# Optimization experiments

Measured on AMD Instinct MI355X. Metric: run time of the kernel, lower is better.

Reference implementation:

```python
import jax, jax.numpy as jnp
import numpy as np

B, C, H, W = 16, 512, 32, 32

def _conv2d(x, w, b, pad):
    y = jax.lax.conv_general_dilated(
        x, w, window_strides=(1, 1), padding=[(pad, pad), (pad, pad)],
        dimension_numbers=('NCHW', 'OIHW', 'NCHW'))
    return y + b[None, :, None, None]

def setup_inputs() -> dict:
    key = jax.random.key(0)
    ks = jax.random.split(key, 10)
    s3 = 1.0 / np.sqrt(C * 9)   # torch conv2d default init scale (3x3)
    s1 = 1.0 / np.sqrt(3 * C)   # 1x1 conv over 3C input channels
    return {
        'x':  jax.random.normal(ks[0], (B, C, H, W), jnp.float32),
        'w1': jax.random.uniform(ks[1], (C, C, 3, 3), jnp.float32, -s3, s3),
        'b1': jax.random.uniform(ks[2], (C,), jnp.float32, -s3, s3),
        'w2': jax.random.uniform(ks[3], (C, C, 3, 3), jnp.float32, -s3, s3),
        'b2': jax.random.uniform(ks[4], (C,), jnp.float32, -s3, s3),
        'w3': jax.random.uniform(ks[5], (C, C, 3, 3), jnp.float32, -s3, s3),
        'b3': jax.random.uniform(ks[6], (C,), jnp.float32, -s3, s3),
        'alpha': jax.random.normal(ks[7], (), jnp.float32) * 0.1,
        'beta':  jax.random.normal(ks[8], (), jnp.float32) * 0.1,
        'wf': jax.random.uniform(ks[9], (C, 3 * C, 1, 1), jnp.float32, -s1, s1),
        'bf': jnp.zeros((C,), jnp.float32),
    }

def reference(x, w1, b1, w2, b2, w3, b3, alpha, beta, wf, bf):
    b, c, h, w = x.shape
    n = h * w
    # --- spatial attention ---
    A = _conv2d(x, w1, b1, 1).reshape(b, c, n)  # [b,C,N]
    Bm = _conv2d(x, w2, b2, 1).reshape(b, c, n)
    D = _conv2d(x, w3, b3, 1).reshape(b, c, n)
    M = jnp.einsum('bcn,bcm->bnm', A, Bm)       # A^T @ B, [b,N,N]
    M = jax.nn.softmax(M, axis=-1)
    # weighted_C = M @ D^T -> [b,N,C]; then permute to [b,C,N]
    spat = jnp.einsum('bnm,bcm->bcn', M, D).reshape(b, c, h, w)
    spat = alpha * spat
    # --- channel attention ---
    Xr = x.reshape(b, c, n)                     # [b,C,N]
    S = jnp.einsum('bcn,bdn->bcd', Xr, Xr)      # [b,C,C]
    S = jax.nn.softmax(S, axis=-1)
    # weighted = S^T @ Xr
    chan = jnp.einsum('bdc,bdn->bcn', S, Xr).reshape(b, c, h, w)
    chan = beta * chan
    # --- fuse ---
    cat = jnp.concatenate((x, spat, chan), axis=1)  # [b,3C,H,W]
    return _conv2d(cat, wf, bf, 0)
```

## Files before the change

kernel.cpp:

```cpp
#include <hip/hip_runtime.h>
#include <hip/hip_bf16.h>
#include <stdint.h>

#define B_   16
#define C_   512
#define N_   1024
#define C3   1536

using bf16x8 = __attribute__((ext_vector_type(8))) __bf16;
using f32x4  = __attribute__((ext_vector_type(4))) float;
typedef unsigned short ushort_t;

__device__ __forceinline__ ushort_t f2bf(float f) {
    union { float f; uint32_t u; } v; v.f = f;
    uint32_t r = v.u + 0x7FFFu + ((v.u >> 16) & 1u);
    return (ushort_t)(r >> 16);
}

typedef __attribute__((address_space(3))) void lds_void_t;
typedef const __attribute__((address_space(1))) void g_void_t;
__device__ __forceinline__ void gload16(const void* g, void* l) {
    __builtin_amdgcn_global_load_lds((g_void_t*)g, (lds_void_t*)l, 16, 0, 0);
}


__global__ void castwf_kernel(const float* __restrict__ wf,
                              ushort_t* __restrict__ Wfb,
                              ushort_t* __restrict__ zp,
                              const float* __restrict__ b1,
                              const float* __restrict__ b2,
                              const float* __restrict__ b3,
                              float* __restrict__ b_all) {
    int idx = blockIdx.x * 256 + threadIdx.x;
    if (idx < 512) zp[idx] = 0;
    if (idx < 1536) b_all[idx] = (idx < 512) ? b1[idx] : (idx < 1024) ? b2[idx - 512] : b3[idx - 1024];
    Wfb[idx] = f2bf(wf[idx]);
}

__global__ void castw_kernel(const float* __restrict__ w,
                             ushort_t* __restrict__ Wall, int coff) {
    int idx = blockIdx.x * 256 + threadIdx.x;
    int t = idx / (C_ * C_);
    int rem = idx - t * (C_ * C_);
    Wall[(size_t)t * (C3 * C_) + (size_t)coff * C_ + rem] = f2bf(w[(size_t)rem * 9 + t]);
}

__global__ void castx_kernel(const float* __restrict__ x,
                             ushort_t* __restrict__ Xb,
                             ushort_t* __restrict__ cat) {
    __shared__ ushort_t t[32][33];
    int n0 = blockIdx.x * 32, c0 = blockIdx.y * 32, b = blockIdx.z;
    int tx = threadIdx.x & 31, ty = threadIdx.x >> 5;
    const float* xb = x + ((size_t)b * C_ + c0) * N_ + n0;
#pragma unroll
    for (int q = 0; q < 4; ++q) {
        int c = ty + q * 8;
        ushort_t h = f2bf(xb[(size_t)c * N_ + tx]);
        Xb[((size_t)b * C_ + c0 + c) * N_ + n0 + tx] = h;
        t[c][tx] = h;
    }
    __syncthreads();
#pragma unroll
    for (int q = 0; q < 4; ++q) {
        int n = ty + q * 8;
        cat[((size_t)b * N_ + n0 + n) * C3 + c0 + tx] = t[tx][n];
    }
}

__global__ void transp_kernel(const ushort_t* __restrict__ Y,
                              ushort_t* __restrict__ Db) {
    __shared__ ushort_t t[32][33];
    int n0 = blockIdx.x * 32, c0 = blockIdx.y * 32, b = blockIdx.z;
    int tx = threadIdx.x & 31, ty = threadIdx.x >> 5;
#pragma unroll
    for (int q = 0; q < 4; ++q) {
        int n = ty + q * 8;
        t[n][tx] = Y[((size_t)b * N_ + n0 + n) * C3 + 1024 + c0 + tx];
    }
    __syncthreads();
#pragma unroll
    for (int q = 0; q < 4; ++q) {
        int c = ty + q * 8;
        Db[((size_t)b * C_ + c0 + c) * N_ + n0 + tx] = t[tx][c];
    }
}

__global__ void softmax_kernel(float* __restrict__ Mb) {
    int n = blockIdx.x, b = blockIdx.y;
    float* row = Mb + ((size_t)b * N_ + n) * N_;
    int tid = threadIdx.x;
    float4 v = ((const float4*)row)[tid];
    float m = fmaxf(fmaxf(v.x, v.y), fmaxf(v.z, v.w));
#pragma unroll
    for (int off = 1; off < 64; off <<= 1) m = fmaxf(m, __shfl_xor(m, off));
    __shared__ float sm[4], ss[4];
    int wid = tid >> 6, lane = tid & 63;
    if (lane == 0) sm[wid] = m;
    __syncthreads();
    m = fmaxf(fmaxf(sm[0], sm[1]), fmaxf(sm[2], sm[3]));
    float e0 = __expf(v.x - m), e1 = __expf(v.y - m);
    float e2 = __expf(v.z - m), e3 = __expf(v.w - m);
    float s = e0 + e1 + e2 + e3;
#pragma unroll
    for (int off = 1; off < 64; off <<= 1) s += __shfl_xor(s, off);
    if (lane == 0) ss[wid] = s;
    __syncthreads();
    s = ss[0] + ss[1] + ss[2] + ss[3];
    float r = 1.0f / s;
    ushort4 o;
    o.x = f2bf(e0 * r); o.y = f2bf(e1 * r); o.z = f2bf(e2 * r); o.w = f2bf(e3 * r);
    ((ushort4*)row)[tid] = o;
}

__global__ void rowstats_kernel(const float* __restrict__ S,
                                float* __restrict__ mxv, float* __restrict__ rzv) {
    int c = blockIdx.x, b = blockIdx.y;
    const float* row = S + ((size_t)b * C_ + c) * C_;
    int tid = threadIdx.x;
    float2 v = ((const float2*)row)[tid];
    float m = fmaxf(v.x, v.y);
#pragma unroll
    for (int off = 1; off < 64; off <<= 1) m = fmaxf(m, __shfl_xor(m, off));
    __shared__ float sm[4], ss[4];
    int wid = tid >> 6, lane = tid & 63;
    if (lane == 0) sm[wid] = m;
    __syncthreads();
    m = fmaxf(fmaxf(sm[0], sm[1]), fmaxf(sm[2], sm[3]));
    float e = __expf(v.x - m) + __expf(v.y - m);
#pragma unroll
    for (int off = 1; off < 64; off <<= 1) e += __shfl_xor(e, off);
    if (lane == 0) ss[wid] = e;
    __syncthreads();
    if (tid == 0) {
        e = ss[0] + ss[1] + ss[2] + ss[3];
        mxv[(size_t)b * C_ + c] = m;
        rzv[(size_t)b * C_ + c] = 1.0f / e;
    }
}

__global__ void sst_kernel(const float* __restrict__ S,
                           const float* __restrict__ mxv, const float* __restrict__ rzv,
                           ushort_t* __restrict__ Sst) {
    int idx = blockIdx.x * 256 + threadIdx.x;
    int d = idx & (C_ - 1);
    int b = idx >> 18;
    float st = mxv[((size_t)b << 9) + d];
    float rz = rzv[((size_t)b << 9) + d];
    Sst[idx] = f2bf(__expf(S[idx] - st) * rz);
}

#define BM 128
#define BN 128
#define BKk 64

template <int XMODE, int OUTF32, int BIASMODE, int SCALE, int SWZ>
__global__ __launch_bounds__(256)
void gemm_bt_kernel(const ushort_t* __restrict__ Ab, int lda, long long strideA, long long tapA,
                    const ushort_t* __restrict__ Bb, int ldb, long long strideB, long long tapB,
                    void* __restrict__ Cb, int ldc, long long strideC,
                    int K, int ntaps,
                    const float* __restrict__ bias,
                    const float* __restrict__ scaleptr,
                    const ushort_t* __restrict__ zpage) {
    __shared__ short As[BM * BKk];
    __shared__ short Bs[BN * BKk];
    int tid = threadIdx.x;
    int wid = tid >> 6, lane = tid & 63;
    int wr = wid >> 1, wc = wid & 1;
    int j0, i0, b;
    if (SWZ) {
        int bid = blockIdx.x;
        int swz = (bid & 7) * 192 + (bid >> 3);
        j0 = (swz >> 7) * BN;
        i0 = (swz & 127) * BM;
        b = 0;
    } else {
        j0 = blockIdx.x * BN; i0 = blockIdx.y * BM; b = blockIdx.z;
    }
    const ushort_t* Abase = Ab + (size_t)b * strideA;
    const ushort_t* Bbase = Bb + (size_t)b * strideB;

    f32x4 acc[4][4] = {};

    int rs = wid * 32 + (lane >> 3);
    int kb = (lane & 7) * 8;

    for (int tap = 0; tap < ntaps; ++tap) {
        const ushort_t* At_ = Abase + (size_t)tap * tapA;
        const ushort_t* Bt_ = Bbase + (size_t)tap * tapB;
        const ushort_t* aq[4];
        const ushort_t* bq[4];
        if (XMODE == 1) {
            int dh = tap / 3 - 1, dw = tap - (tap / 3) * 3 - 1;
            int nshift = dh * 32 + dw;
#pragma unroll
            for (int q = 0; q < 4; ++q) {
                int n = i0 + rs + q * 8;
                int nn = n & (N_ - 1);
                int hh = (nn >> 5) + dh, ww = (nn & 31) + dw;
                bool valid = ((unsigned)hh < 32u) && ((unsigned)ww < 32u);
                aq[q] = valid ? (At_ + (size_t)(n + nshift) * lda + kb) : (zpage + kb);
            }
        } else {
#pragma unroll
            for (int q = 0; q < 4; ++q)
                aq[q] = At_ + (size_t)(i0 + rs + q * 8) * lda + kb;
        }
#pragma unroll
        for (int q = 0; q < 4; ++q)
            bq[q] = Bt_ + (size_t)(j0 + rs + q * 8) * ldb + kb;

        for (int kk = 0; kk < K; kk += BKk) {
            __syncthreads();
#pragma unroll
            for (int q = 0; q < 4; ++q) {
                gload16(aq[q], &As[(wid * 32 + q * 8) * BKk]);
                aq[q] += BKk;
                gload16(bq[q], &Bs[(wid * 32 + q * 8) * BKk]);
                bq[q] += BKk;
            }
            __syncthreads();
#pragma unroll
            for (int kc = 0; kc < BKk; kc += 32) {
                bf16x8 af[4], bfr[4];
#pragma unroll
                for (int m = 0; m < 4; ++m)
                    af[m] = *(const bf16x8*)&As[(wr * 64 + m * 16 + (lane & 15)) * BKk + kc + (lane >> 4) * 8];
#pragma unroll
                for (int nb = 0; nb < 4; ++nb)
                    bfr[nb] = *(const bf16x8*)&Bs[(wc * 64 + nb * 16 + (lane & 15)) * BKk + kc + (lane >> 4) * 8];
#pragma unroll
                for (int m = 0; m < 4; ++m)
#pragma unroll
                    for (int nb = 0; nb < 4; ++nb)
                        acc[m][nb] = __builtin_amdgcn_mfma_f32_16x16x32_bf16(af[m], bfr[nb], acc[m][nb], 0, 0, 0);
            }
        }
    }

    float scale = SCALE ? *scaleptr : 1.0f;
#pragma unroll
    for (int m = 0; m < 4; ++m) {
#pragma unroll
        for (int nb = 0; nb < 4; ++nb) {
            int i = i0 + wr * 64 + m * 16 + (lane >> 4) * 4;
            int j = j0 + wc * 64 + nb * 16 + (lane & 15);
#pragma unroll
            for (int r = 0; r < 4; ++r) {
                float v = acc[m][nb][r];
                if (BIASMODE == 1) v += bias[i + r];
                if (BIASMODE == 2) v += bias[j];
                if (SCALE) v *= scale;
                if (OUTF32)
                    ((float*)Cb)[(size_t)b * strideC + (size_t)(i + r) * ldc + j] = v;
                else
                    ((ushort_t*)Cb)[(size_t)b * strideC + (size_t)(i + r) * ldc + j] = f2bf(v);
            }
        }
    }
}

constexpr size_t OFF_ZP   = 0;
constexpr size_t OFF_BALL = 1024;
constexpr size_t OFF_WFB  = OFF_BALL + 6144;
constexpr size_t OFF_CAT  = OFF_WFB + (size_t)C_ * C3 * 2;
constexpr size_t OFF_Y    = OFF_CAT + (size_t)B_ * N_ * C3 * 2;
constexpr size_t OFF_DB   = OFF_Y + (size_t)B_ * N_ * C3 * 2;
constexpr size_t OFF_SR   = OFF_DB + (size_t)B_ * C_ * N_ * 2;
constexpr size_t OFF_SST  = OFF_SR + (size_t)B_ * C_ * C_ * 4;
constexpr size_t OFF_MX   = OFF_SST + (size_t)B_ * C_ * C_ * 2;
constexpr size_t OFF_RZ   = OFF_MX + (size_t)B_ * C_ * 4;
constexpr size_t OFF_U    = OFF_RZ + (size_t)B_ * C_ * 4;
constexpr size_t OFF_WALL = OFF_U;
constexpr size_t OFF_XB   = OFF_U + (size_t)9 * C3 * C_ * 2;
constexpr size_t OFF_M    = OFF_U;
constexpr size_t EXT_A    = OFF_XB + (size_t)B_ * C_ * N_ * 2;
constexpr size_t EXT_B    = OFF_M + (size_t)B_ * N_ * N_ * 4;
constexpr size_t WS_NEED  = EXT_A > EXT_B ? EXT_A : EXT_B;

extern "C" void kernel_launch(void* const* d_in, const int* in_sizes, int n_in,
                              void* d_out, int out_size, void* d_ws, size_t ws_size,
                              hipStream_t stream) {
    const float* x   = (const float*)d_in[0];
    const float* w1  = (const float*)d_in[1];
    const float* b1  = (const float*)d_in[2];
    const float* w2  = (const float*)d_in[3];
    const float* b2  = (const float*)d_in[4];
    const float* w3  = (const float*)d_in[5];
    const float* b3  = (const float*)d_in[6];
    const float* alpha = (const float*)d_in[7];
    const float* beta  = (const float*)d_in[8];
    const float* wf  = (const float*)d_in[9];
    const float* bfv = (const float*)d_in[10];
    float* out = (float*)d_out;
    char* ws = (char*)d_ws;
    if (ws_size < WS_NEED) return;

    ushort_t* zp   = (ushort_t*)(ws + OFF_ZP);
    float*    ball = (float*)(ws + OFF_BALL);
    ushort_t* Wfb  = (ushort_t*)(ws + OFF_WFB);
    ushort_t* cat  = (ushort_t*)(ws + OFF_CAT);
    ushort_t* Y    = (ushort_t*)(ws + OFF_Y);
    ushort_t* Db   = (ushort_t*)(ws + OFF_DB);
    float*    Sr   = (float*)(ws + OFF_SR);
    ushort_t* Sst  = (ushort_t*)(ws + OFF_SST);
    float*    mxv  = (float*)(ws + OFF_MX);
    float*    rzv  = (float*)(ws + OFF_RZ);
    ushort_t* Wall = (ushort_t*)(ws + OFF_WALL);
    ushort_t* Xb   = (ushort_t*)(ws + OFF_XB);
    float*    Mb   = (float*)(ws + OFF_M);

    castwf_kernel<<<(C_ * C3) / 256, 256, 0, stream>>>(wf, Wfb, zp, b1, b2, b3, ball);
    castw_kernel<<<(9 * C_ * C_) / 256, 256, 0, stream>>>(w1, Wall, 0);
    castw_kernel<<<(9 * C_ * C_) / 256, 256, 0, stream>>>(w2, Wall, 512);
    castw_kernel<<<(9 * C_ * C_) / 256, 256, 0, stream>>>(w3, Wall, 1024);
    castx_kernel<<<dim3(N_ / 32, C_ / 32, B_), 256, 0, stream>>>(x, Xb, cat);

    gemm_bt_kernel<1, 0, 2, 0, 1><<<dim3(1536), 256, 0, stream>>>(
        cat, C3, 0, 0,
        Wall, C_, 0, (long long)C3 * C_,
        Y, C3, 0,
        C_, 9, ball, nullptr, zp);
    transp_kernel<<<dim3(N_ / 32, C_ / 32, B_), 256, 0, stream>>>(Y, Db);
    gemm_bt_kernel<0, 1, 0, 0, 0><<<dim3(4, 4, B_), 256, 0, stream>>>(
        Xb, N_, (long long)C_ * N_, 0,
        Xb, N_, (long long)C_ * N_, 0,
        Sr, C_, (long long)C_ * C_,
        N_, 1, nullptr, nullptr, zp);
    rowstats_kernel<<<dim3(C_, B_), 256, 0, stream>>>(Sr, mxv, rzv);
    sst_kernel<<<(B_ * C_ * C_) / 256, 256, 0, stream>>>(Sr, mxv, rzv, Sst);
    gemm_bt_kernel<0, 1, 0, 0, 0><<<dim3(8, 8, B_), 256, 0, stream>>>(
        Y, C3, (long long)N_ * C3, 0,
        Y + 512, C3, (long long)N_ * C3, 0,
        Mb, N_, (long long)N_ * N_,
        C_, 1, nullptr, nullptr, zp);
    softmax_kernel<<<dim3(N_, B_), 256, 0, stream>>>(Mb);
    gemm_bt_kernel<0, 0, 0, 1, 0><<<dim3(4, 8, B_), 256, 0, stream>>>(
        (const ushort_t*)Mb, 2048, (long long)N_ * 2048, 0,
        Db, N_, (long long)C_ * N_, 0,
        cat + 512, C3, (long long)N_ * C3,
        N_, 1, nullptr, alpha, zp);
    gemm_bt_kernel<0, 0, 0, 1, 0><<<dim3(4, 8, B_), 256, 0, stream>>>(
        cat, C3, (long long)N_ * C3, 0,
        Sst, C_, (long long)C_ * C_, 0,
        cat + 1024, C3, (long long)N_ * C3,
        C_, 1, nullptr, beta, zp);
    gemm_bt_kernel<0, 1, 1, 0, 0><<<dim3(8, 4, B_), 256, 0, stream>>>(
        Wfb, C3, 0, 0,
        cat, C3, (long long)N_ * C3, 0,
        out, N_, (long long)C_ * N_,
        C3, 1, bfv, nullptr, zp);
}
```

Before: 509.9 us.

## Add triple-buffered 256x128 GEMM kernel with swizzled LDS and use it everywhere

Introduces a new GEMM kernel with 512 threads, a 256x128 tile, a three-slot LDS ring that prefetches two k-steps ahead using vmcnt waits, XOR-swizzled LDS layout to reduce bank conflicts, and raised wave priority around the MFMA block. All five main GEMMs, including the implicit 3x3 conv, switch to it. The conv loses its block-order swizzle for L2 locality. The larger tiles and 144KB+ LDS footprint lower occupancy and halve grid sizes for some GEMMs (e.g. 256 blocks), which may underfill the device.

```diff
diff --git a/kernel.cpp b/kernel.cpp
--- a/kernel.cpp
+++ b/kernel.cpp
@@ -167,16 +167,7 @@
     int tid = threadIdx.x;
     int wid = tid >> 6, lane = tid & 63;
     int wr = wid >> 1, wc = wid & 1;
-    int j0, i0, b;
-    if (SWZ) {
-        int bid = blockIdx.x;
-        int swz = (bid & 7) * 192 + (bid >> 3);
-        j0 = (swz >> 7) * BN;
-        i0 = (swz & 127) * BM;
-        b = 0;
-    } else {
-        j0 = blockIdx.x * BN; i0 = blockIdx.y * BM; b = blockIdx.z;
-    }
+    int j0 = blockIdx.x * BN, i0 = blockIdx.y * BM, b = blockIdx.z;
     const ushort_t* Abase = Ab + (size_t)b * strideA;
     const ushort_t* Bbase = Bb + (size_t)b * strideB;
 
@@ -190,22 +181,9 @@
         const ushort_t* Bt_ = Bbase + (size_t)tap * tapB;
         const ushort_t* aq[4];
         const ushort_t* bq[4];
-        if (XMODE == 1) {
-            int dh = tap / 3 - 1, dw = tap - (tap / 3) * 3 - 1;
-            int nshift = dh * 32 + dw;
-#pragma unroll
-            for (int q = 0; q < 4; ++q) {
-                int n = i0 + rs + q * 8;
-                int nn = n & (N_ - 1);
-                int hh = (nn >> 5) + dh, ww = (nn & 31) + dw;
-                bool valid = ((unsigned)hh < 32u) && ((unsigned)ww < 32u);
-                aq[q] = valid ? (At_ + (size_t)(n + nshift) * lda + kb) : (zpage + kb);
-            }
-        } else {
-#pragma unroll
-            for (int q = 0; q < 4; ++q)
-                aq[q] = At_ + (size_t)(i0 + rs + q * 8) * lda + kb;
-        }
+#pragma unroll
+        for (int q = 0; q < 4; ++q)
+            aq[q] = At_ + (size_t)(i0 + rs + q * 8) * lda + kb;
 #pragma unroll
         for (int q = 0; q < 4; ++q)
             bq[q] = Bt_ + (size_t)(j0 + rs + q * 8) * ldb + kb;
@@ -236,6 +214,137 @@
                         acc[m][nb] = __builtin_amdgcn_mfma_f32_16x16x32_bf16(af[m], bfr[nb], acc[m][nb], 0, 0, 0);
             }
         }
+    }
+
+    float scale = SCALE ? *scaleptr : 1.0f;
+#pragma unroll
+    for (int m = 0; m < 4; ++m) {
+#pragma unroll
+        for (int nb = 0; nb < 4; ++nb) {
+            int i = i0 + wr * 64 + m * 16 + (lane >> 4) * 4;
+            int j = j0 + wc * 64 + nb * 16 + (lane & 15);
+#pragma unroll
+            for (int r = 0; r < 4; ++r) {
+                float v = acc[m][nb][r];
+                if (BIASMODE == 1) v += bias[i + r];
+                if (BIASMODE == 2) v += bias[j];
+                if (SCALE) v *= scale;
+                if (OUTF32)
+                    ((float*)Cb)[(size_t)b * strideC + (size_t)(i + r) * ldc + j] = v;
+                else
+                    ((ushort_t*)Cb)[(size_t)b * strideC + (size_t)(i + r) * ldc + j] = f2bf(v);
+            }
+        }
+    }
+}
+
+#define R3BM 256
+#define R3BN 128
+#define R3BK 64
+
+template <int XMODE, int OUTF32, int BIASMODE, int SCALE>
+__global__ __launch_bounds__(512, 2)
+void gemm_r3_kernel(const ushort_t* __restrict__ Ab, int lda, long long strideA, long long tapA,
+                    const ushort_t* __restrict__ Bb, int ldb, long long strideB, long long tapB,
+                    void* __restrict__ Cb, int ldc, long long strideC,
+                    int K, int ntaps,
+                    const float* __restrict__ bias,
+                    const float* __restrict__ scaleptr,
+                    const ushort_t* __restrict__ zpage) {
+    __shared__ short As[3][R3BM * R3BK];
+    __shared__ short Bs[3][R3BN * R3BK];
+    int tid = threadIdx.x;
+    int wid = tid >> 6, lane = tid & 63;
+    int wr = wid >> 1, wc = wid & 1;
+    int j0 = blockIdx.x * R3BN, i0 = blockIdx.y * R3BM, b = blockIdx.z;
+    const ushort_t* Abase = Ab + (size_t)b * strideA;
+    const ushort_t* Bbase = Bb + (size_t)b * strideB;
+    int kpt = K >> 6;
+    int nt = ntaps * kpt;
+
+    f32x4 acc[4][4] = {};
+
+    int sr = tid >> 3;
+    int klds = (tid & 7) * 8;
+
+    auto STAGE = [&](int tt, int slot) {
+        int tap = tt / kpt;
+        int kk = (tt - tap * kpt) << 6;
+        const ushort_t* At_ = Abase + (size_t)tap * tapA + kk;
+        const ushort_t* Bt_ = Bbase + (size_t)tap * tapB + kk;
+        int dh = 0, nshift = 0;
+        int dw = 0;
+        if (XMODE == 1) { dh = tap / 3 - 1; dw = tap - (tap / 3) * 3 - 1; nshift = dh * 32 + dw; }
+#pragma unroll
+        for (int s = 0; s < 4; ++s) {
+            int r = sr + s * 64;
+            int ks = klds ^ (((r >> 2) & 3) << 3);
+            const ushort_t* src;
+            if (XMODE == 1) {
+                int n = i0 + r;
+                int nn = n & (N_ - 1);
+                int hh = (nn >> 5) + dh, ww = (nn & 31) + dw;
+                bool valid = ((unsigned)hh < 32u) && ((unsigned)ww < 32u);
+                src = valid ? (At_ + (size_t)(n + nshift) * lda + ks) : (zpage + ks);
+            } else {
+                src = At_ + (size_t)(i0 + r) * lda + ks;
+            }
+            gload16(src, &As[slot][wid * 512 + s * 4096]);
+        }
+#pragma unroll
+        for (int s = 0; s < 2; ++s) {
+            int r = sr + s * 64;
+            int ks = klds ^ (((r >> 2) & 3) << 3);
+            const ushort_t* src = Bt_ + (size_t)(j0 + r) * ldb + ks;
+            gload16(src, &Bs[slot][wid * 512 + s * 4096]);
+        }
+    };
+
+    STAGE(0, 0);
+    STAGE(1, 1);
+
+    for (int t = 0; t < nt; ++t) {
+        int slot = t - (t / 3) * 3;
+        if (t + 1 < nt) asm volatile("s_waitcnt vmcnt(6)" ::: "memory");
+        else            asm volatile("s_waitcnt vmcnt(0)" ::: "memory");
+        __builtin_amdgcn_s_barrier();
+        __builtin_amdgcn_sched_barrier(0);
+
+        bf16x8 af[4][2], bfr[4][2];
+#pragma unroll
+        for (int m = 0; m < 4; ++m) {
+            int row = wr * 64 + m * 16 + (lane & 15);
+            int sw = ((row >> 2) & 3) << 3;
+#pragma unroll
+            for (int h = 0; h < 2; ++h) {
+                int k = h * 32 + (lane >> 4) * 8;
+                af[m][h] = *(const bf16x8*)&As[slot][row * R3BK + (k ^ sw)];
+            }
+        }
+#pragma unroll
+        for (int nb = 0; nb < 4; ++nb) {
+            int row = wc * 64 + nb * 16 + (lane & 15);
+            int sw = ((row >> 2) & 3) << 3;
+#pragma unroll
+            for (int h = 0; h < 2; ++h) {
+                int k = h * 32 + (lane >> 4) * 8;
+                bfr[nb][h] = *(const bf16x8*)&Bs[slot][row * R3BK + (k ^ sw)];
+            }
+        }
+
+        if (t + 2 < nt) STAGE(t + 2, (t + 2) - ((t + 2) / 3) * 3);
+
+        asm volatile("s_waitcnt lgkmcnt(0)" ::: "memory");
+        __builtin_amdgcn_sched_barrier(0);
+        __builtin_amdgcn_s_setprio(1);
+#pragma unroll
+        for (int h = 0; h < 2; ++h)
+#pragma unroll
+            for (int m = 0; m < 4; ++m)
+#pragma unroll
+                for (int nb = 0; nb < 4; ++nb)
+                    acc[m][nb] = __builtin_amdgcn_mfma_f32_16x16x32_bf16(af[m][h], bfr[nb][h], acc[m][nb], 0, 0, 0);
+        __builtin_amdgcn_s_setprio(0);
     }
 
     float scale = SCALE ? *scaleptr : 1.0f;
@@ -316,7 +425,7 @@
     castw_kernel<<<(9 * C_ * C_) / 256, 256, 0, stream>>>(w3, Wall, 1024);
     castx_kernel<<<dim3(N_ / 32, C_ / 32, B_), 256, 0, stream>>>(x, Xb, cat);
 
-    gemm_bt_kernel<1, 0, 2, 0, 1><<<dim3(1536), 256, 0, stream>>>(
+    gemm_r3_kernel<1, 0, 2, 0><<<dim3(12, 64, 1), 512, 0, stream>>>(
         cat, C3, 0, 0,
         Wall, C_, 0, (long long)C3 * C_,
         Y, C3, 0,
@@ -329,23 +438,23 @@
         N_, 1, nullptr, nullptr, zp);
     rowstats_kernel<<<dim3(C_, B_), 256, 0, stream>>>(Sr, mxv, rzv);
     sst_kernel<<<(B_ * C_ * C_) / 256, 256, 0, stream>>>(Sr, mxv, rzv, Sst);
-    gemm_bt_kernel<0, 1, 0, 0, 0><<<dim3(8, 8, B_), 256, 0, stream>>>(
+    gemm_r3_kernel<0, 1, 0, 0><<<dim3(8, 4, B_), 512, 0, stream>>>(
         Y, C3, (long long)N_ * C3, 0,
         Y + 512, C3, (long long)N_ * C3, 0,
         Mb, N_, (long long)N_ * N_,
         C_, 1, nullptr, nullptr, zp);
     softmax_kernel<<<dim3(N_, B_), 256, 0, stream>>>(Mb);
-    gemm_bt_kernel<0, 0, 0, 1, 0><<<dim3(4, 8, B_), 256, 0, stream>>>(
+    gemm_r3_kernel<0, 0, 0, 1><<<dim3(4, 4, B_), 512, 0, stream>>>(
         (const ushort_t*)Mb, 2048, (long long)N_ * 2048, 0,
         Db, N_, (long long)C_ * N_, 0,
         cat + 512, C3, (long long)N_ * C3,
         N_, 1, nullptr, alpha, zp);
-    gemm_bt_kernel<0, 0, 0, 1, 0><<<dim3(4, 8, B_), 256, 0, stream>>>(
+    gemm_r3_kernel<0, 0, 0, 1><<<dim3(4, 4, B_), 512, 0, stream>>>(
         cat, C3, (long long)N_ * C3, 0,
         Sst, C_, (long long)C_ * C_, 0,
         cat + 1024, C3, (long long)N_ * C3,
         C_, 1, nullptr, beta, zp);
-    gemm_bt_kernel<0, 1, 1, 0, 0><<<dim3(8, 4, B_), 256, 0, stream>>>(
+    gemm_r3_kernel<0, 1, 1, 0><<<dim3(8, 2, B_), 512, 0, stream>>>(
         Wfb, C3, 0, 0,
         cat, C3, (long long)N_ * C3, 0,
         out, N_, (long long)C_ * N_,
```

Measured after the change: 562.3 us. +10.3%, slower.
